# Optimization experiments

Hardware: AMD Instinct MI355X
Metric: run time of the kernel (lower is better)

The kernel has to match this reference:

```python
import jax, jax.numpy as jnp
import numpy as np

G, NG, K, D = 64, 2048, 16, 256  # graphs, nodes/graph, eigvecs/graph, feature dim


def setup_inputs() -> dict:
    key = jax.random.key(0)
    k0, k1, k2, k3, k4 = jax.random.split(key, 5)
    x = jax.random.normal(k0, (G * NG, D), jnp.float32)
    # eigenvectors of per-graph Laplacians (values arbitrary for correctness baseline)
    eigvec = jax.random.normal(k1, (G * NG, K), jnp.float32) / np.float32(np.sqrt(NG))
    split_real = jnp.ones((D,), jnp.float32)
    split_imag = jnp.ones((D,), jnp.float32)
    spec_filter = jax.random.uniform(k2, (G, K, D), dtype=jnp.float32)
    W1 = jax.random.normal(k3, (D, D), jnp.float32) / np.float32(np.sqrt(D))
    W2 = jax.random.normal(k4, (D, D), jnp.float32) / np.float32(np.sqrt(D))
    factor_split = jnp.ones((D, 2), jnp.float32)
    return dict(x=x, eigvec=eigvec, split_real=split_real, split_imag=split_imag,
                spec_filter=spec_filter, W1=W1, W2=W2, factor_split=factor_split)


def _silu_norm(h):
    # SiLU gating: sigmoid of complex L2-norm over the spectral (k) axis, keepdim
    norm = jnp.sqrt(jnp.sum(h.real ** 2 + h.imag ** 2, axis=1, keepdims=True))
    return h * jax.nn.sigmoid(norm)


def reference(x, eigvec, split_real, split_imag, spec_filter, W1, W2, factor_split):
    # SpecFeatureTransformLayer (split variant): x -> complex
    xc = jax.lax.complex(split_real * x, split_imag * x)      # [N, D] complex64
    V = eigvec.reshape(G, NG, K)                              # block-diagonal eigvec basis
    xg = xc.reshape(G, NG, D)
    # eigvec^H @ x  (block-diag COO matmul, eigvecs real so conj is a no-op)
    x_spec = jnp.einsum('gnk,gnd->gkd', V, xg)                # [G, K, D] complex64
    x_spec = spec_filter * x_spec                             # learned spectral filter
    # silu_stack: MaybeComplexLinear (same real weight on real & imag) + norm-gated SiLU
    for W in (W1, W2):                                        # W: [out, in], y = x @ W^T
        h = jnp.einsum('gkd,ed->gke', x_spec, W)
        x_spec = _silu_norm(h)
    # project back to node domain: eigvec @ x_spec
    xn = jnp.einsum('gnk,gkd->gnd', V, x_spec).reshape(G * NG, D)
    # real/imag merge via factor_split
    out = xn.real * factor_split[:, 0] + xn.imag * factor_split[:, 1]
    return out + x                                            # node residual
```

## Files before the change

kernel.cpp:

```cpp
#include <hip/hip_runtime.h>
#include <math.h>

#define G  64
#define NG 2048
#define K  16
#define D  256
#define KD (K*D)
#define CHUNK 128

typedef float v4f __attribute__((ext_vector_type(4)));

__device__ __forceinline__ int rfl(int v) { return __builtin_amdgcn_readfirstlane(v); }

__global__ __launch_bounds__(256) void k_project(const float* __restrict__ x,
                                                 const float* __restrict__ eig,
                                                 float* __restrict__ P) {
    __shared__ float red[2 * KD];
    const int b  = blockIdx.x;
    const int g  = b >> 4, c = b & 15;
    const int n0 = g * NG + c * CHUNK;
    const int t  = threadIdx.x;
    const int d4 = t & 63;
    const int nq = t >> 6;

    float acc[K][4];
#pragma unroll
    for (int k = 0; k < K; ++k)
#pragma unroll
        for (int j = 0; j < 4; ++j) acc[k][j] = 0.f;

    const float4* x4 = (const float4*)x;
#pragma unroll 4
    for (int nn = 0; nn < CHUNK / 4; ++nn) {
        const int un = rfl(n0 + nq * (CHUNK / 4) + nn);
        const float* vr = eig + (size_t)un * K;
        const float4 xv = x4[(size_t)un * 64 + d4];
#pragma unroll
        for (int k = 0; k < K; ++k) {
            const float vk = vr[k];
            acc[k][0] += vk * xv.x; acc[k][1] += vk * xv.y;
            acc[k][2] += vk * xv.z; acc[k][3] += vk * xv.w;
        }
    }

    if (nq >= 2) {
#pragma unroll
        for (int k = 0; k < K; ++k)
            *(float4*)&red[(nq - 2) * KD + k * D + d4 * 4] =
                make_float4(acc[k][0], acc[k][1], acc[k][2], acc[k][3]);
    }
    __syncthreads();
    if (nq < 2) {
#pragma unroll
        for (int k = 0; k < K; ++k) {
            const float4 r = *(const float4*)&red[nq * KD + k * D + d4 * 4];
            acc[k][0] += r.x; acc[k][1] += r.y; acc[k][2] += r.z; acc[k][3] += r.w;
        }
    }
    __syncthreads();
    if (nq == 1) {
#pragma unroll
        for (int k = 0; k < K; ++k)
            *(float4*)&red[k * D + d4 * 4] =
                make_float4(acc[k][0], acc[k][1], acc[k][2], acc[k][3]);
    }
    __syncthreads();
    if (nq == 0) {
        float* Pg = P + (size_t)g * KD;
#pragma unroll
        for (int k = 0; k < K; ++k) {
            const float4 r = *(const float4*)&red[k * D + d4 * 4];
            atomicAdd(Pg + k * D + d4 * 4 + 0, acc[k][0] + r.x);
            atomicAdd(Pg + k * D + d4 * 4 + 1, acc[k][1] + r.y);
            atomicAdd(Pg + k * D + d4 * 4 + 2, acc[k][2] + r.z);
            atomicAdd(Pg + k * D + d4 * 4 + 3, acc[k][3] + r.w);
        }
    }
}

template <int LAYER>
__global__ __launch_bounds__(256) void k_mlp(const float* __restrict__ A,
                                             const float* __restrict__ B,
                                             const float* __restrict__ sr,
                                             const float* __restrict__ si,
                                             const float* __restrict__ W,
                                             const float* __restrict__ fs,
                                             float* __restrict__ o0,
                                             float* __restrict__ o1) {
    __shared__ float sXr[KD];
    __shared__ float sXi[KD];
    __shared__ float sRed[2 * 4 * K * 64];
    const int g     = blockIdx.x >> 2;
    const int slice = blockIdx.x & 3;
    const int t     = threadIdx.x;

    if (LAYER == 1) {
        for (int idx = t; idx < KD; idx += 256) {
            const int d = idx & (D - 1);
            const float base = A[(size_t)g * KD + idx] * B[(size_t)g * KD + idx];
            sXr[idx] = base * sr[d];
            sXi[idx] = base * si[d];
        }
    } else {
        const float4* a4 = (const float4*)(A + (size_t)g * KD);
        const float4* b4 = (const float4*)(B + (size_t)g * KD);
        float4* xr4 = (float4*)sXr;
        float4* xi4 = (float4*)sXi;
        for (int idx = t; idx < KD / 4; idx += 256) { xr4[idx] = a4[idx]; xi4[idx] = b4[idx]; }
    }
    __syncthreads();

    const int el = t & 63;
    const int e  = slice * 64 + el;
    const int dq = t >> 6;

    float pr[K], pi[K];
#pragma unroll
    for (int k = 0; k < K; ++k) { pr[k] = 0.f; pi[k] = 0.f; }

    const float4* w4 = (const float4*)(W + (size_t)e * D);
    for (int ds = dq * 16; ds < dq * 16 + 16; ++ds) {
        const float4 w = w4[ds];
        const int d0 = ds * 4;
#pragma unroll
        for (int k = 0; k < K; ++k) {
            const float4 xr = *(const float4*)&sXr[k * D + d0];
            const float4 xi = *(const float4*)&sXi[k * D + d0];
            pr[k] += xr.x * w.x + xr.y * w.y + xr.z * w.z + xr.w * w.w;
            pi[k] += xi.x * w.x + xi.y * w.y + xi.z * w.z + xi.w * w.w;
        }
    }
    __syncthreads();
#pragma unroll
    for (int k = 0; k < K; ++k) {
        sRed[((0 * 4 + dq) * K + k) * 64 + el] = pr[k];
        sRed[((1 * 4 + dq) * K + k) * 64 + el] = pi[k];
    }
    __syncthreads();

    if (t < 64) {
        float hr[K], hi[K];
        float nrm = 0.f;
#pragma unroll
        for (int k = 0; k < K; ++k) {
            float r = 0.f, im = 0.f;
#pragma unroll
            for (int w = 0; w < 4; ++w) {
                r  += sRed[((0 * 4 + w) * K + k) * 64 + t];
                im += sRed[((1 * 4 + w) * K + k) * 64 + t];
            }
            hr[k] = r; hi[k] = im;
            nrm += r * r + im * im;
        }
        const float sg = 1.f / (1.f + expf(-sqrtf(nrm)));
        const int eg = slice * 64 + t;
        if (LAYER == 1) {
#pragma unroll
            for (int k = 0; k < K; ++k) {
                o0[((size_t)g * K + k) * D + eg] = hr[k] * sg;
                o1[((size_t)g * K + k) * D + eg] = hi[k] * sg;
            }
        } else {
            const float f0 = fs[eg * 2], f1 = fs[eg * 2 + 1];
#pragma unroll
            for (int k = 0; k < K; ++k)
                o0[((size_t)g * K + k) * D + eg] = (hr[k] * sg) * f0 + (hi[k] * sg) * f1;
        }
    }
}

__global__ __launch_bounds__(256) void k_back(const float* __restrict__ x,
                                              const float* __restrict__ eig,
                                              const float* __restrict__ z,
                                              float* __restrict__ out) {
    const int b  = blockIdx.x;
    const int g  = b >> 4, c = b & 15;
    const int n0 = g * NG + c * CHUNK;
    const int t  = threadIdx.x;
    const int d4 = t & 63;
    const int nq = t >> 6;

    float zr[K][4];
    const float4* z4 = (const float4*)(z + (size_t)g * KD);
#pragma unroll
    for (int k = 0; k < K; ++k) {
        const float4 zv = z4[k * 64 + d4];
        zr[k][0] = zv.x; zr[k][1] = zv.y; zr[k][2] = zv.z; zr[k][3] = zv.w;
    }

    const float4* x4 = (const float4*)x;
    v4f* o4 = (v4f*)out;
#pragma unroll 4
    for (int nn = 0; nn < CHUNK / 4; ++nn) {
        const int un = rfl(n0 + nq * (CHUNK / 4) + nn);
        const float* vr = eig + (size_t)un * K;
        const size_t idx = (size_t)un * 64 + d4;
        float4 o = x4[idx];
#pragma unroll
        for (int k = 0; k < K; ++k) {
            const float vk = vr[k];
            o.x += vk * zr[k][0]; o.y += vk * zr[k][1];
            o.z += vk * zr[k][2]; o.w += vk * zr[k][3];
        }
        v4f ov; ov.x = o.x; ov.y = o.y; ov.z = o.z; ov.w = o.w;
        __builtin_nontemporal_store(ov, &o4[idx]);
    }
}

extern "C" void kernel_launch(void* const* d_in, const int* in_sizes, int n_in,
                              void* d_out, int out_size, void* d_ws, size_t ws_size,
                              hipStream_t stream) {
    const float* x    = (const float*)d_in[0];
    const float* eig  = (const float*)d_in[1];
    const float* sr   = (const float*)d_in[2];
    const float* si   = (const float*)d_in[3];
    const float* filt = (const float*)d_in[4];
    const float* W1   = (const float*)d_in[5];
    const float* W2   = (const float*)d_in[6];
    const float* fs   = (const float*)d_in[7];
    float* out = (float*)d_out;

    float* P   = (float*)d_ws;
    float* y1r = P + (size_t)G * KD;
    float* y1i = y1r + (size_t)G * KD;
    float* z   = P;

    (void)hipMemsetAsync(P, 0, (size_t)G * KD * sizeof(float), stream);
    k_project<<<G * 16, 256, 0, stream>>>(x, eig, P);
    k_mlp<1><<<G * 4, 256, 0, stream>>>(P, filt, sr, si, W1, nullptr, y1r, y1i);
    k_mlp<2><<<G * 4, 256, 0, stream>>>(y1r, y1i, nullptr, nullptr, W2, fs, z, nullptr);
    k_back<<<G * 16, 256, 0, stream>>>(x, eig, z, out);
}
```

Measured before the change: 357.9 us.

## Replace atomic projection with per-chunk partials, separate reduce kernel, and smem-staged eigvecs

The projection kernel now runs 64-thread blocks over 32-row chunks, stages eigenvector rows in shared memory, and writes per-chunk partial sums to scratch instead of doing atomics. A new reduce kernel sums the partials and applies the filter and split scaling. The MLP kernels stage W slices in XOR-swizzled shared memory and read X directly from global memory. The back-projection also stages eigvecs in shared memory. Partials and intermediates are stored in the output buffer as scratch, which adds extra global traffic but removes the memset and atomic contention.

```diff
diff --git a/kernel.cpp b/kernel.cpp
--- a/kernel.cpp
+++ b/kernel.cpp
@@ -6,22 +6,28 @@
 #define K  16
 #define D  256
 #define KD (K*D)
-#define CHUNK 128
+#define ROWS 32
+#define NCHUNK (NG/ROWS)
+#define WPF ((size_t)G * NCHUNK * KD)
 
 typedef float v4f __attribute__((ext_vector_type(4)));
 
-__device__ __forceinline__ int rfl(int v) { return __builtin_amdgcn_readfirstlane(v); }
-
-__global__ __launch_bounds__(256) void k_project(const float* __restrict__ x,
-                                                 const float* __restrict__ eig,
-                                                 float* __restrict__ P) {
-    __shared__ float red[2 * KD];
+__global__ __launch_bounds__(64) void k_project(const float* __restrict__ x,
+                                                const float* __restrict__ eig,
+                                                float* __restrict__ WP) {
+    __shared__ float sV[ROWS * K];
     const int b  = blockIdx.x;
-    const int g  = b >> 4, c = b & 15;
-    const int n0 = g * NG + c * CHUNK;
+    const int g  = b >> 6, c = b & 63;
+    const int n0 = g * NG + c * ROWS;
     const int t  = threadIdx.x;
-    const int d4 = t & 63;
-    const int nq = t >> 6;
+
+    {
+        const float4* e4 = (const float4*)(eig + (size_t)n0 * K);
+        float4* s4 = (float4*)sV;
+        s4[t]      = e4[t];
+        s4[t + 64] = e4[t + 64];
+    }
+    __syncthreads();
 
     float acc[K][4];
 #pragma unroll
@@ -29,112 +35,107 @@
 #pragma unroll
         for (int j = 0; j < 4; ++j) acc[k][j] = 0.f;
 
-    const float4* x4 = (const float4*)x;
+    const float4* x4 = (const float4*)x + (size_t)n0 * 64;
 #pragma unroll 4
-    for (int nn = 0; nn < CHUNK / 4; ++nn) {
-        const int un = rfl(n0 + nq * (CHUNK / 4) + nn);
-        const float* vr = eig + (size_t)un * K;
-        const float4 xv = x4[(size_t)un * 64 + d4];
-#pragma unroll
-        for (int k = 0; k < K; ++k) {
-            const float vk = vr[k];
-            acc[k][0] += vk * xv.x; acc[k][1] += vk * xv.y;
-            acc[k][2] += vk * xv.z; acc[k][3] += vk * xv.w;
-        }
-    }
-
-    if (nq >= 2) {
-#pragma unroll
-        for (int k = 0; k < K; ++k)
-            *(float4*)&red[(nq - 2) * KD + k * D + d4 * 4] =
-                make_float4(acc[k][0], acc[k][1], acc[k][2], acc[k][3]);
-    }
-    __syncthreads();
-    if (nq < 2) {
-#pragma unroll
-        for (int k = 0; k < K; ++k) {
-            const float4 r = *(const float4*)&red[nq * KD + k * D + d4 * 4];
-            acc[k][0] += r.x; acc[k][1] += r.y; acc[k][2] += r.z; acc[k][3] += r.w;
-        }
-    }
-    __syncthreads();
-    if (nq == 1) {
-#pragma unroll
-        for (int k = 0; k < K; ++k)
-            *(float4*)&red[k * D + d4 * 4] =
-                make_float4(acc[k][0], acc[k][1], acc[k][2], acc[k][3]);
-    }
-    __syncthreads();
-    if (nq == 0) {
-        float* Pg = P + (size_t)g * KD;
-#pragma unroll
-        for (int k = 0; k < K; ++k) {
-            const float4 r = *(const float4*)&red[k * D + d4 * 4];
-            atomicAdd(Pg + k * D + d4 * 4 + 0, acc[k][0] + r.x);
-            atomicAdd(Pg + k * D + d4 * 4 + 1, acc[k][1] + r.y);
-            atomicAdd(Pg + k * D + d4 * 4 + 2, acc[k][2] + r.z);
-            atomicAdd(Pg + k * D + d4 * 4 + 3, acc[k][3] + r.w);
-        }
-    }
+    for (int n = 0; n < ROWS; ++n) {
+        const float4 xv = x4[n * 64 + t];
+#pragma unroll
+        for (int kq = 0; kq < 4; ++kq) {
+            const float4 v = *(const float4*)&sV[n * K + kq * 4];
+            acc[kq*4+0][0] += v.x * xv.x; acc[kq*4+0][1] += v.x * xv.y;
+            acc[kq*4+0][2] += v.x * xv.z; acc[kq*4+0][3] += v.x * xv.w;
+            acc[kq*4+1][0] += v.y * xv.x; acc[kq*4+1][1] += v.y * xv.y;
+            acc[kq*4+1][2] += v.y * xv.z; acc[kq*4+1][3] += v.y * xv.w;
+            acc[kq*4+2][0] += v.z * xv.x; acc[kq*4+2][1] += v.z * xv.y;
+            acc[kq*4+2][2] += v.z * xv.z; acc[kq*4+2][3] += v.z * xv.w;
+            acc[kq*4+3][0] += v.w * xv.x; acc[kq*4+3][1] += v.w * xv.y;
+            acc[kq*4+3][2] += v.w * xv.z; acc[kq*4+3][3] += v.w * xv.w;
+        }
+    }
+
+    float4* wp4 = (float4*)WP + (size_t)b * (KD / 4);
+#pragma unroll
+    for (int k = 0; k < K; ++k)
+        wp4[k * 64 + t] = make_float4(acc[k][0], acc[k][1], acc[k][2], acc[k][3]);
+}
+
+__global__ __launch_bounds__(256) void k_reduce(const float* __restrict__ WP,
+                                                const float* __restrict__ filt,
+                                                const float* __restrict__ sr,
+                                                const float* __restrict__ si,
+                                                float* __restrict__ Xr,
+                                                float* __restrict__ Xi) {
+    const int b = blockIdx.x;
+    const int g = b >> 2, q = b & 3;
+    const int f = q * 256 + threadIdx.x;
+    const float4* wp4 = (const float4*)WP + (size_t)g * NCHUNK * (KD / 4);
+    float ax = 0.f, ay = 0.f, az = 0.f, aw = 0.f;
+#pragma unroll 8
+    for (int w = 0; w < NCHUNK; ++w) {
+        const float4 p = wp4[(size_t)w * (KD / 4) + f];
+        ax += p.x; ay += p.y; az += p.z; aw += p.w;
+    }
+    const float4 fl = ((const float4*)filt)[(size_t)g * (KD / 4) + f];
+    const int d4 = f & 63;
+    const float4 s0 = ((const float4*)sr)[d4];
+    const float4 s1 = ((const float4*)si)[d4];
+    float4 xr, xi;
+    xr.x = ax * fl.x * s0.x; xr.y = ay * fl.y * s0.y;
+    xr.z = az * fl.z * s0.z; xr.w = aw * fl.w * s0.w;
+    xi.x = ax * fl.x * s1.x; xi.y = ay * fl.y * s1.y;
+    xi.z = az * fl.z * s1.z; xi.w = aw * fl.w * s1.w;
+    ((float4*)Xr)[(size_t)g * (KD / 4) + f] = xr;
+    ((float4*)Xi)[(size_t)g * (KD / 4) + f] = xi;
 }
 
 template <int LAYER>
-__global__ __launch_bounds__(256) void k_mlp(const float* __restrict__ A,
-                                             const float* __restrict__ B,
-                                             const float* __restrict__ sr,
-                                             const float* __restrict__ si,
+__global__ __launch_bounds__(256) void k_mlp(const float* __restrict__ Xr,
+                                             const float* __restrict__ Xi,
                                              const float* __restrict__ W,
                                              const float* __restrict__ fs,
                                              float* __restrict__ o0,
                                              float* __restrict__ o1) {
-    __shared__ float sXr[KD];
-    __shared__ float sXi[KD];
-    __shared__ float sRed[2 * 4 * K * 64];
-    const int g     = blockIdx.x >> 2;
-    const int slice = blockIdx.x & 3;
+    __shared__ float4 sW[64 * 64];
+    __shared__ float  sRed[4 * 64 * 8];
+    const int b     = blockIdx.x;
+    const int g     = b >> 2;
+    const int slice = b & 3;
     const int t     = threadIdx.x;
 
-    if (LAYER == 1) {
-        for (int idx = t; idx < KD; idx += 256) {
-            const int d = idx & (D - 1);
-            const float base = A[(size_t)g * KD + idx] * B[(size_t)g * KD + idx];
-            sXr[idx] = base * sr[d];
-            sXi[idx] = base * si[d];
-        }
-    } else {
-        const float4* a4 = (const float4*)(A + (size_t)g * KD);
-        const float4* b4 = (const float4*)(B + (size_t)g * KD);
-        float4* xr4 = (float4*)sXr;
-        float4* xi4 = (float4*)sXi;
-        for (int idx = t; idx < KD / 4; idx += 256) { xr4[idx] = a4[idx]; xi4[idx] = b4[idx]; }
+    {
+        const float4* Wg = (const float4*)W + (size_t)slice * 64 * 64;
+#pragma unroll
+        for (int it = 0; it < 16; ++it) {
+            const int idx = it * 256 + t;
+            const int e = idx >> 6, ds = idx & 63;
+            sW[e * 64 + (ds ^ (e & 7))] = Wg[idx];
+        }
     }
     __syncthreads();
 
     const int el = t & 63;
-    const int e  = slice * 64 + el;
-    const int dq = t >> 6;
-
-    float pr[K], pi[K];
-#pragma unroll
-    for (int k = 0; k < K; ++k) { pr[k] = 0.f; pi[k] = 0.f; }
-
-    const float4* w4 = (const float4*)(W + (size_t)e * D);
-    for (int ds = dq * 16; ds < dq * 16 + 16; ++ds) {
-        const float4 w = w4[ds];
-        const int d0 = ds * 4;
-#pragma unroll
-        for (int k = 0; k < K; ++k) {
-            const float4 xr = *(const float4*)&sXr[k * D + d0];
-            const float4 xi = *(const float4*)&sXi[k * D + d0];
-            pr[k] += xr.x * w.x + xr.y * w.y + xr.z * w.z + xr.w * w.w;
-            pi[k] += xi.x * w.x + xi.y * w.y + xi.z * w.z + xi.w * w.w;
-        }
-    }
-    __syncthreads();
-#pragma unroll
-    for (int k = 0; k < K; ++k) {
-        sRed[((0 * 4 + dq) * K + k) * 64 + el] = pr[k];
-        sRed[((1 * 4 + dq) * K + k) * 64 + el] = pi[k];
+    const int kq = t >> 6;
+    const float* xr = Xr + (size_t)g * KD + (kq * 4) * D;
+    const float* xi = Xi + (size_t)g * KD + (kq * 4) * D;
+
+    float pr[4] = {0.f, 0.f, 0.f, 0.f};
+    float pi[4] = {0.f, 0.f, 0.f, 0.f};
+#pragma unroll 4
+    for (int ds = 0; ds < 64; ++ds) {
+        const float4 w = sW[el * 64 + (ds ^ (el & 7))];
+#pragma unroll
+        for (int kk = 0; kk < 4; ++kk) {
+            const float4 a = *(const float4*)&xr[kk * D + ds * 4];
+            const float4 c = *(const float4*)&xi[kk * D + ds * 4];
+            pr[kk] += w.x * a.x + w.y * a.y + w.z * a.z + w.w * a.w;
+            pi[kk] += w.x * c.x + w.y * c.y + w.z * c.z + w.w * c.w;
+        }
+    }
+
+#pragma unroll
+    for (int kk = 0; kk < 4; ++kk) {
+        sRed[(kq * 64 + el) * 8 + kk]     = pr[kk];
+        sRed[(kq * 64 + el) * 8 + 4 + kk] = pi[kk];
     }
     __syncthreads();
 
@@ -142,68 +143,67 @@
         float hr[K], hi[K];
         float nrm = 0.f;
 #pragma unroll
-        for (int k = 0; k < K; ++k) {
-            float r = 0.f, im = 0.f;
-#pragma unroll
-            for (int w = 0; w < 4; ++w) {
-                r  += sRed[((0 * 4 + w) * K + k) * 64 + t];
-                im += sRed[((1 * 4 + w) * K + k) * 64 + t];
+        for (int q2 = 0; q2 < 4; ++q2)
+#pragma unroll
+            for (int kk = 0; kk < 4; ++kk) {
+                const float r  = sRed[(q2 * 64 + t) * 8 + kk];
+                const float im = sRed[(q2 * 64 + t) * 8 + 4 + kk];
+                hr[q2 * 4 + kk] = r; hi[q2 * 4 + kk] = im;
+                nrm += r * r + im * im;
             }
-            hr[k] = r; hi[k] = im;
-            nrm += r * r + im * im;
-        }
         const float sg = 1.f / (1.f + expf(-sqrtf(nrm)));
-        const int eg = slice * 64 + t;
+        const int e = slice * 64 + t;
         if (LAYER == 1) {
 #pragma unroll
             for (int k = 0; k < K; ++k) {
-                o0[((size_t)g * K + k) * D + eg] = hr[k] * sg;
-                o1[((size_t)g * K + k) * D + eg] = hi[k] * sg;
+                o0[(size_t)g * KD + k * D + e] = hr[k] * sg;
+                o1[(size_t)g * KD + k * D + e] = hi[k] * sg;
             }
         } else {
-            const float f0 = fs[eg * 2], f1 = fs[eg * 2 + 1];
+            const float f0 = fs[e * 2], f1 = fs[e * 2 + 1];
 #pragma unroll
             for (int k = 0; k < K; ++k)
-                o0[((size_t)g * K + k) * D + eg] = (hr[k] * sg) * f0 + (hi[k] * sg) * f1;
-        }
-    }
-}
-
-__global__ __launch_bounds__(256) void k_back(const float* __restrict__ x,
-                                              const float* __restrict__ eig,
-                                              const float* __restrict__ z,
-                                              float* __restrict__ out) {
+                o0[(size_t)g * KD + k * D + e] = (hr[k] * sg) * f0 + (hi[k] * sg) * f1;
+        }
+    }
+}
+
+__global__ __launch_bounds__(64) void k_back(const float* __restrict__ x,
+                                             const float* __restrict__ eig,
+                                             const float* __restrict__ z,
+                                             float* __restrict__ out) {
+    __shared__ float sV[ROWS * K];
     const int b  = blockIdx.x;
-    const int g  = b >> 4, c = b & 15;
-    const int n0 = g * NG + c * CHUNK;
+    const int g  = b >> 6, c = b & 63;
+    const int n0 = g * NG + c * ROWS;
     const int t  = threadIdx.x;
-    const int d4 = t & 63;
-    const int nq = t >> 6;
-
-    float zr[K][4];
-    const float4* z4 = (const float4*)(z + (size_t)g * KD);
-#pragma unroll
-    for (int k = 0; k < K; ++k) {
-        const float4 zv = z4[k * 64 + d4];
-        zr[k][0] = zv.x; zr[k][1] = zv.y; zr[k][2] = zv.z; zr[k][3] = zv.w;
-    }
-
-    const float4* x4 = (const float4*)x;
-    v4f* o4 = (v4f*)out;
+    {
+        const float4* e4 = (const float4*)(eig + (size_t)n0 * K);
+        float4* s4 = (float4*)sV;
+        s4[t]      = e4[t];
+        s4[t + 64] = e4[t + 64];
+    }
+    float4 zr[K];
+    const float4* z4 = (const float4*)z + (size_t)g * (KD / 4);
+#pragma unroll
+    for (int k = 0; k < K; ++k) zr[k] = z4[k * 64 + t];
+    __syncthreads();
+
+    const float4* x4 = (const float4*)x + (size_t)n0 * 64;
+    v4f* o4 = (v4f*)out + (size_t)n0 * 64;
 #pragma unroll 4
-    for (int nn = 0; nn < CHUNK / 4; ++nn) {
-        const int un = rfl(n0 + nq * (CHUNK / 4) + nn);
-        const float* vr = eig + (size_t)un * K;
-        const size_t idx = (size_t)un * 64 + d4;
-        float4 o = x4[idx];
-#pragma unroll
-        for (int k = 0; k < K; ++k) {
-            const float vk = vr[k];
-            o.x += vk * zr[k][0]; o.y += vk * zr[k][1];
-            o.z += vk * zr[k][2]; o.w += vk * zr[k][3];
+    for (int n = 0; n < ROWS; ++n) {
+        float4 o = x4[n * 64 + t];
+#pragma unroll
+        for (int kq = 0; kq < 4; ++kq) {
+            const float4 v = *(const float4*)&sV[n * K + kq * 4];
+            o.x += v.x * zr[kq*4+0].x + v.y * zr[kq*4+1].x + v.z * zr[kq*4+2].x + v.w * zr[kq*4+3].x;
+            o.y += v.x * zr[kq*4+0].y + v.y * zr[kq*4+1].y + v.z * zr[kq*4+2].y + v.w * zr[kq*4+3].y;
+            o.z += v.x * zr[kq*4+0].z + v.y * zr[kq*4+1].z + v.z * zr[kq*4+2].z + v.w * zr[kq*4+3].z;
+            o.w += v.x * zr[kq*4+0].w + v.y * zr[kq*4+1].w + v.z * zr[kq*4+2].w + v.w * zr[kq*4+3].w;
         }
         v4f ov; ov.x = o.x; ov.y = o.y; ov.z = o.z; ov.w = o.w;
-        __builtin_nontemporal_store(ov, &o4[idx]);
+        __builtin_nontemporal_store(ov, &o4[n * 64 + t]);
     }
 }
 
@@ -220,14 +220,16 @@
     const float* fs   = (const float*)d_in[7];
     float* out = (float*)d_out;
 
-    float* P   = (float*)d_ws;
-    float* y1r = P + (size_t)G * KD;
+    float* WP  = out;
+    float* Xr  = out + WPF;
+    float* Xi  = Xr + (size_t)G * KD;
+    float* y1r = Xi + (size_t)G * KD;
     float* y1i = y1r + (size_t)G * KD;
-    float* z   = P;
-
-    (void)hipMemsetAsync(P, 0, (size_t)G * KD * sizeof(float), stream);
-    k_project<<<G * 16, 256, 0, stream>>>(x, eig, P);
-    k_mlp<1><<<G * 4, 256, 0, stream>>>(P, filt, sr, si, W1, nullptr, y1r, y1i);
-    k_mlp<2><<<G * 4, 256, 0, stream>>>(y1r, y1i, nullptr, nullptr, W2, fs, z, nullptr);
-    k_back<<<G * 16, 256, 0, stream>>>(x, eig, z, out);
-}
+    float* z   = (float*)d_ws;
+
+    k_project<<<G * NCHUNK, 64, 0, stream>>>(x, eig, WP);
+    k_reduce<<<G * 4, 256, 0, stream>>>(WP, filt, sr, si, Xr, Xi);
+    k_mlp<1><<<G * 4, 256, 0, stream>>>(Xr, Xi, W1, nullptr, y1r, y1i);
+    k_mlp<2><<<G * 4, 256, 0, stream>>>(y1r, y1i, W2, fs, z, nullptr);
+    k_back<<<G * NCHUNK, 64, 0, stream>>>(x, eig, z, out);
+}
```

New measurement: 339.0 us. 5.3% less time.
